# Optimization experiments

Hardware: AMD Instinct MI355X
Metric: run time of the kernel (lower is better)

Reference implementation:

```python
import jax, jax.numpy as jnp
import numpy as np

B, T, C = 4, 2048, 1024
N_HEAD = 16
HEAD = C // N_HEAD  # 64


def setup_inputs() -> dict:
    key = jax.random.key(0)
    k1, k2, k3 = jax.random.split(key, 3)
    x = jax.random.normal(k1, (B, T, C), dtype=jnp.float32)
    w_attn = jax.random.normal(k2, (C, 3 * C), dtype=jnp.float32) * (1.0 / np.sqrt(C))
    w_proj = jax.random.normal(k3, (C, C), dtype=jnp.float32) * (1.0 / np.sqrt(C))
    return {"x": x, "w_attn": w_attn, "w_proj": w_proj}


def reference(x, w_attn, w_proj):
    b, t, c = x.shape
    qkv = x @ w_attn  # [B,T,3C]
    q, k, v = jnp.split(qkv, 3, axis=-1)
    # [B,T,H,D] -> [B,H,T,D]
    q = q.reshape(b, t, N_HEAD, HEAD).transpose(0, 2, 1, 3)
    k = k.reshape(b, t, N_HEAD, HEAD).transpose(0, 2, 1, 3)
    v = v.reshape(b, t, N_HEAD, HEAD).transpose(0, 2, 1, 3)
    scale = 1.0 / np.sqrt(HEAD).astype(np.float32)
    attn = jnp.einsum('bhqd,bhkd->bhqk', q, k) * scale  # [B,H,T,T]
    causal = jnp.tril(jnp.ones((t, t), dtype=bool))
    attn = jnp.where(causal[None, None], attn, -jnp.inf)
    sm = jax.nn.softmax(attn, axis=-1)
    out = jnp.einsum('bhqk,bhkd->bhqd', sm, v)  # [B,H,T,D]
    out = out.transpose(0, 2, 1, 3).reshape(b, t, c)
    return out @ w_proj
```

## Files before the change

### kernel.cpp

```cpp
#include <hip/hip_runtime.h>
#include <stdint.h>

typedef unsigned short u16;
typedef __bf16 bf16x8 __attribute__((ext_vector_type(8)));
typedef float f32x4 __attribute__((ext_vector_type(4)));
typedef float f32x16 __attribute__((ext_vector_type(16)));

#define B_ 4
#define T_ 2048
#define C_ 1024
#define NH_ 16
#define HD_ 64
#define M_ (B_ * T_)
#define N1_ (3 * C_)
#define NQK_ 2048

__device__ inline u16 f2bf(float f) {
    uint32_t u = __float_as_uint(f);
    u += 0x7FFFu + ((u >> 16) & 1u);
    return (u16)(u >> 16);
}

__device__ inline bf16x8 ld_bf16x8(const u16* p) {
    return *(const bf16x8*)(const void*)p;
}

__device__ inline uint32_t cvtpk_bf16(float a, float b) {
    uint32_t r;
    asm("v_cvt_pk_bf16_f32 %0, %1, %2" : "=v"(r) : "v"(a), "v"(b));
    return r;
}

__device__ inline float exp2_fast(float x) {
    float r;
    asm("v_exp_f32 %0, %1" : "=v"(r) : "v"(x));
    return r;
}

__device__ inline void gload16(const u16* g, u16* l) {
    __builtin_amdgcn_global_load_lds(
        (const __attribute__((address_space(1))) uint32_t*)g,
        (__attribute__((address_space(3))) uint32_t*)l, 16, 0, 0);
}

__global__ void f32_to_bf16_k(const float* __restrict__ in, u16* __restrict__ out, int n) {
    int i = (blockIdx.x * blockDim.x + threadIdx.x) * 4;
    int stride = gridDim.x * blockDim.x * 4;
    for (; i < n; i += stride) {
        float4 v = *(const float4*)(in + i);
        uint2 o;
        o.x = (uint32_t)f2bf(v.x) | ((uint32_t)f2bf(v.y) << 16);
        o.y = (uint32_t)f2bf(v.z) | ((uint32_t)f2bf(v.w) << 16);
        *(uint2*)(out + i) = o;
    }
}

__global__ void transpose_f32_bf16_k(const float* __restrict__ in, u16* __restrict__ out,
                                     int R, int Cc, int scaleRows, float scale) {
    __shared__ float tile[32][33];
    int c0 = blockIdx.x * 32, r0 = blockIdx.y * 32;
    int tx = threadIdx.x, ty = threadIdx.y;
#pragma unroll
    for (int i = 0; i < 4; ++i)
        tile[ty + i * 8][tx] = in[(size_t)(r0 + ty + i * 8) * Cc + c0 + tx];
    __syncthreads();
#pragma unroll
    for (int i = 0; i < 4; ++i) {
        int orow = c0 + ty + i * 8;
        float v = tile[tx][ty + i * 8];
        if (orow < scaleRows) v *= scale;
        out[(size_t)orow * R + r0 + tx] = f2bf(v);
    }
}

template <int MODE>
__global__ __launch_bounds__(256) void gemm_bt_k(const u16* __restrict__ A,
                                                 const u16* __restrict__ Bt,
                                                 void* __restrict__ Cp,
                                                 u16* __restrict__ Vp,
                                                 int M, int N, int K) {
    __shared__ u16 As[3][128 * 32];
    __shared__ u16 Bs[3][128 * 32];
    const int t = threadIdx.x;
    const int w = t >> 6, l = t & 63;
    const int wr = w >> 1, wc = w & 1;
    const int lr = l & 15, lg = l >> 4;
    const int bid = blockIdx.x;
    const int xcd = bid & 7, j = bid >> 3;
    const int mt = xcd * 8 + (j & 7);
    const int nt = j >> 3;
    const int R0 = mt * 128, C0 = nt * 128;

    const int sr = t >> 2;
    const int sc = (((t & 3) ^ ((t >> 3) & 3)) * 8);
    const u16* Ag  = A  + (size_t)(R0 + sr) * K + sc;
    const u16* Ag2 = Ag + (size_t)64 * K;
    const u16* Bg  = Bt + (size_t)(C0 + sr) * K + sc;
    const u16* Bg2 = Bg + (size_t)64 * K;

    f32x4 acc[4][4] = {};
    const int nk = K / 32;

#define STAGE(KT, BI)                                               \
    do {                                                            \
        gload16(Ag  + (size_t)(KT) * 32, As[BI] + t * 8);           \
        gload16(Ag2 + (size_t)(KT) * 32, As[BI] + t * 8 + 2048);    \
        gload16(Bg  + (size_t)(KT) * 32, Bs[BI] + t * 8);           \
        gload16(Bg2 + (size_t)(KT) * 32, Bs[BI] + t * 8 + 2048);    \
    } while (0)

    STAGE(0, 0);
    if (nk > 1) STAGE(1, 1);

    const int lg8 = (lg * 8) ^ (((lr >> 1) & 3) * 8);

    int bi = 0;
    for (int kt = 0; kt < nk; ++kt) {
        if (kt + 1 < nk) asm volatile("s_waitcnt vmcnt(4)" ::: "memory");
        else             asm volatile("s_waitcnt vmcnt(0)" ::: "memory");
        __builtin_amdgcn_s_barrier();
        __builtin_amdgcn_sched_barrier(0);
        if (kt + 2 < nk) {
            int bn = bi + 2; if (bn >= 3) bn -= 3;
            STAGE(kt + 2, bn);
        }

        const u16* Ab = As[bi];
        const u16* Bb = Bs[bi];
        bf16x8 af[4], bfr[4];
#pragma unroll
        for (int mi = 0; mi < 4; ++mi)
            af[mi] = ld_bf16x8(Ab + (wr * 64 + mi * 16 + lr) * 32 + lg8);
#pragma unroll
        for (int nj = 0; nj < 4; ++nj)
            bfr[nj] = ld_bf16x8(Bb + (wc * 64 + nj * 16 + lr) * 32 + lg8);
        __builtin_amdgcn_s_setprio(1);
#pragma unroll
        for (int mi = 0; mi < 4; ++mi)
#pragma unroll
            for (int nj = 0; nj < 4; ++nj)
                acc[mi][nj] = __builtin_amdgcn_mfma_f32_16x16x32_bf16(af[mi], bfr[nj],
                                                                      acc[mi][nj], 0, 0, 0);
        __builtin_amdgcn_s_setprio(0);
        bi = (bi + 1 == 3) ? 0 : bi + 1;
    }
#undef STAGE

    if (MODE == 2 && C0 >= 2048) {
#pragma unroll
        for (int mi = 0; mi < 4; ++mi) {
            int row = R0 + wr * 64 + mi * 16 + lg * 4;
            int bb = row >> 11, tt = row & 2047;
#pragma unroll
            for (int nj = 0; nj < 4; ++nj) {
                int cv = C0 - 2048 + wc * 64 + nj * 16 + lr;
                int hh = cv >> 6, dd = cv & 63;
                ushort4 pk;
                pk.x = f2bf(acc[mi][nj][0]);
                pk.y = f2bf(acc[mi][nj][1]);
                pk.z = f2bf(acc[mi][nj][2]);
                pk.w = f2bf(acc[mi][nj][3]);
                *(ushort4*)(Vp + (((size_t)bb * NH_ + hh) * HD_ + dd) * (size_t)T_ + tt) = pk;
            }
        }
    } else {
#pragma unroll
        for (int mi = 0; mi < 4; ++mi) {
            int row = R0 + wr * 64 + mi * 16 + lg * 4;
#pragma unroll
            for (int nj = 0; nj < 4; ++nj) {
                int col = C0 + wc * 64 + nj * 16 + lr;
#pragma unroll
                for (int r = 0; r < 4; ++r) {
                    if (MODE == 0)
                        ((float*)Cp)[(size_t)(row + r) * N + col] = acc[mi][nj][r];
                    else
                        ((u16*)Cp)[(size_t)(row + r) * NQK_ + col] = f2bf(acc[mi][nj][r]);
                }
            }
        }
    }
}

__global__ __launch_bounds__(256, 3) void attn_fwd_k(const u16* __restrict__ qk,
                                                     const u16* __restrict__ vT,
                                                     u16* __restrict__ attO) {
    __shared__ u16 Ks[2][64 * 64];
    __shared__ u16 Vs[2][64 * 64];

    const int t = threadIdx.x;
    const int w = t >> 6, l = t & 63;
    const int r0 = l & 31, hi = l >> 5;
    const int lin = blockIdx.x;
    const int bh = (lin & 7) * 8 + ((lin >> 3) & 7);
    const int J = 15 - (lin >> 6);
    const int b = bh >> 4, h = bh & 15;
    const u16* qkB = qk + (size_t)b * T_ * NQK_;

    const int sr = t >> 3;
    const int sof = ((t & 7) * 8) ^ ((sr & 7) << 3);
    const u16* gK = qkB + (size_t)sr * NQK_ + C_ + h * HD_ + sof;
    const u16* gV = vT + ((size_t)bh * HD_ + sr) * (size_t)T_ + sof;

    const int qW = J * 128 + w * 32;
    const int nt = 2 * J + 2;

    bf16x8 qf[4];
    {
        const u16* qp = qkB + (size_t)(qW + r0) * NQK_ + h * HD_ + hi * 8;
#pragma unroll
        for (int dc = 0; dc < 4; ++dc) qf[dc] = ld_bf16x8(qp + dc * 16);
    }

    f32x16 acc0 = {}, acc1 = {};
    float m = -1e30f, lsum = 0.f;

    gload16(gK, Ks[0] + t * 8);
    gload16(gK + (size_t)32 * NQK_, Ks[0] + t * 8 + 2048);
    gload16(gV, Vs[0] + t * 8);
    gload16(gV + (size_t)32 * T_, Vs[0] + t * 8 + 2048);
    __syncthreads();

    for (int kt = 0; kt < nt; ++kt) {
        const int kv = kt * 64;
        if (kt + 1 < nt) {
            u16* dK = Ks[(kt + 1) & 1];
            u16* dV = Vs[(kt + 1) & 1];
            gload16(gK + (size_t)(kv + 64) * NQK_, dK + t * 8);
            gload16(gK + (size_t)(kv + 96) * NQK_, dK + t * 8 + 2048);
            gload16(gV + (kv + 64), dV + t * 8);
            gload16(gV + (size_t)32 * T_ + (kv + 64), dV + t * 8 + 2048);
        }
        const u16* Kb = Ks[kt & 1];
        const u16* Vb = Vs[kt & 1];

        if (kv <= qW) {
            const bool diag = (kv + 64 > qW);
            const bool up = (!diag) || (w & 1);

            f32x16 s0 = {}, s1 = {};
            __builtin_amdgcn_s_setprio(1);
#pragma unroll
            for (int dc = 0; dc < 4; ++dc) {
                int off = (dc * 32 + hi * 16) ^ ((r0 & 7) << 4);
                bf16x8 k0 = ld_bf16x8((const u16*)((const char*)Kb + r0 * 128 + off));
                s0 = __builtin_amdgcn_mfma_f32_32x32x16_bf16(k0, qf[dc], s0, 0, 0, 0);
                if (up) {
                    bf16x8 k1 = ld_bf16x8((const u16*)((const char*)Kb + r0 * 128 + 4096 + off));
                    s1 = __builtin_amdgcn_mfma_f32_32x32x16_bf16(k1, qf[dc], s1, 0, 0, 0);
                }
            }
            __builtin_amdgcn_s_setprio(0);

            if (diag) {
                int qrel = qW + r0 - kv;
#pragma unroll
                for (int rg = 0; rg < 16; ++rg) {
                    int kv0 = (rg & 3) + 8 * (rg >> 2) + hi * 4;
                    s0[rg] = (kv0 > qrel) ? -1e30f : s0[rg];
                    if (up) s1[rg] = (kv0 + 32 > qrel) ? -1e30f : s1[rg];
                }
            }

            float a4[8];
            if (up) {
#pragma unroll
                for (int i = 0; i < 8; ++i)
                    a4[i] = fmaxf(fmaxf(s0[i], s0[i + 8]), fmaxf(s1[i], s1[i + 8]));
            } else {
#pragma unroll
                for (int i = 0; i < 8; ++i) a4[i] = fmaxf(s0[i], s0[i + 8]);
            }
#pragma unroll
            for (int i = 0; i < 4; ++i) a4[i] = fmaxf(a4[i], a4[i + 4]);
            float mx = fmaxf(fmaxf(a4[0], a4[1]), fmaxf(a4[2], a4[3]));
            mx = fmaxf(mx, __shfl_xor(mx, 32));

            if (!__all(mx - m <= 8.f)) {
                float mn = fmaxf(m, mx);
                float corr = exp2_fast(m - mn);
                m = mn;
                lsum *= corr;
#pragma unroll
                for (int rg = 0; rg < 16; ++rg) { acc0[rg] *= corr; acc1[rg] *= corr; }
            }
#pragma unroll
            for (int rg = 0; rg < 16; ++rg) s0[rg] = exp2_fast(s0[rg] - m);
            if (up) {
#pragma unroll
                for (int rg = 0; rg < 16; ++rg) s1[rg] = exp2_fast(s1[rg] - m);
            }
            float sb[8];
            if (up) {
#pragma unroll
                for (int i = 0; i < 8; ++i) sb[i] = (s0[i] + s0[i + 8]) + (s1[i] + s1[i + 8]);
            } else {
#pragma unroll
                for (int i = 0; i < 8; ++i) sb[i] = s0[i] + s0[i + 8];
            }
#pragma unroll
            for (int i = 0; i < 4; ++i) sb[i] += sb[i + 4];
            float rs = (sb[0] + sb[1]) + (sb[2] + sb[3]);
            rs += __shfl_xor(rs, 32);
            lsum += rs;

            bf16x8 pb0, pb1, pb2, pb3;
            {
                uint32_t c0 = cvtpk_bf16(s0[0], s0[1]),   c1 = cvtpk_bf16(s0[2], s0[3]);
                uint32_t c2 = cvtpk_bf16(s0[4], s0[5]),   c3 = cvtpk_bf16(s0[6], s0[7]);
                uint32_t c4 = cvtpk_bf16(s0[8], s0[9]),   c5 = cvtpk_bf16(s0[10], s0[11]);
                uint32_t c6 = cvtpk_bf16(s0[12], s0[13]), c7 = cvtpk_bf16(s0[14], s0[15]);
                uint32_t x0 = (uint32_t)__shfl_xor((int)c0, 32), x1 = (uint32_t)__shfl_xor((int)c1, 32);
                uint32_t x2 = (uint32_t)__shfl_xor((int)c2, 32), x3 = (uint32_t)__shfl_xor((int)c3, 32);
                uint32_t x4 = (uint32_t)__shfl_xor((int)c4, 32), x5 = (uint32_t)__shfl_xor((int)c5, 32);
                uint32_t x6 = (uint32_t)__shfl_xor((int)c6, 32), x7 = (uint32_t)__shfl_xor((int)c7, 32);
                union { uint32_t u[4]; bf16x8 v; } f0, f1;
                f0.u[0] = hi ? x2 : c0;  f0.u[1] = hi ? x3 : c1;
                f0.u[2] = hi ? c2 : x0;  f0.u[3] = hi ? c3 : x1;
                f1.u[0] = hi ? x6 : c4;  f1.u[1] = hi ? x7 : c5;
                f1.u[2] = hi ? c6 : x4;  f1.u[3] = hi ? c7 : x5;
                pb0 = f0.v; pb1 = f1.v;
            }
            if (up) {
                uint32_t c0 = cvtpk_bf16(s1[0], s1[1]),   c1 = cvtpk_bf16(s1[2], s1[3]);
                uint32_t c2 = cvtpk_bf16(s1[4], s1[5]),   c3 = cvtpk_bf16(s1[6], s1[7]);
                uint32_t c4 = cvtpk_bf16(s1[8], s1[9]),   c5 = cvtpk_bf16(s1[10], s1[11]);
                uint32_t c6 = cvtpk_bf16(s1[12], s1[13]), c7 = cvtpk_bf16(s1[14], s1[15]);
                uint32_t x0 = (uint32_t)__shfl_xor((int)c0, 32), x1 = (uint32_t)__shfl_xor((int)c1, 32);
                uint32_t x2 = (uint32_t)__shfl_xor((int)c2, 32), x3 = (uint32_t)__shfl_xor((int)c3, 32);
                uint32_t x4 = (uint32_t)__shfl_xor((int)c4, 32), x5 = (uint32_t)__shfl_xor((int)c5, 32);
                uint32_t x6 = (uint32_t)__shfl_xor((int)c6, 32), x7 = (uint32_t)__shfl_xor((int)c7, 32);
                union { uint32_t u[4]; bf16x8 v; } f0, f1;
                f0.u[0] = hi ? x2 : c0;  f0.u[1] = hi ? x3 : c1;
                f0.u[2] = hi ? c2 : x0;  f0.u[3] = hi ? c3 : x1;
                f1.u[0] = hi ? x6 : c4;  f1.u[1] = hi ? x7 : c5;
                f1.u[2] = hi ? c6 : x4;  f1.u[3] = hi ? c7 : x5;
                pb2 = f0.v; pb3 = f1.v;
            }

            __builtin_amdgcn_s_setprio(1);
            {
                int off0 = (hi * 16) ^ ((r0 & 7) << 4);
                int off1 = (32 + hi * 16) ^ ((r0 & 7) << 4);
                bf16x8 va0 = ld_bf16x8((const u16*)((const char*)Vb + r0 * 128 + off0));
                bf16x8 va1 = ld_bf16x8((const u16*)((const char*)Vb + r0 * 128 + off1));
                bf16x8 vb0 = ld_bf16x8((const u16*)((const char*)Vb + r0 * 128 + 4096 + off0));
                bf16x8 vb1 = ld_bf16x8((const u16*)((const char*)Vb + r0 * 128 + 4096 + off1));
                acc0 = __builtin_amdgcn_mfma_f32_32x32x16_bf16(va0, pb0, acc0, 0, 0, 0);
                acc0 = __builtin_amdgcn_mfma_f32_32x32x16_bf16(va1, pb1, acc0, 0, 0, 0);
                acc1 = __builtin_amdgcn_mfma_f32_32x32x16_bf16(vb0, pb0, acc1, 0, 0, 0);
                acc1 = __builtin_amdgcn_mfma_f32_32x32x16_bf16(vb1, pb1, acc1, 0, 0, 0);
                if (up) {
                    int off2 = (64 + hi * 16) ^ ((r0 & 7) << 4);
                    int off3 = (96 + hi * 16) ^ ((r0 & 7) << 4);
                    bf16x8 va2 = ld_bf16x8((const u16*)((const char*)Vb + r0 * 128 + off2));
                    bf16x8 va3 = ld_bf16x8((const u16*)((const char*)Vb + r0 * 128 + off3));
                    bf16x8 vb2 = ld_bf16x8((const u16*)((const char*)Vb + r0 * 128 + 4096 + off2));
                    bf16x8 vb3 = ld_bf16x8((const u16*)((const char*)Vb + r0 * 128 + 4096 + off3));
                    acc0 = __builtin_amdgcn_mfma_f32_32x32x16_bf16(va2, pb2, acc0, 0, 0, 0);
                    acc0 = __builtin_amdgcn_mfma_f32_32x32x16_bf16(va3, pb3, acc0, 0, 0, 0);
                    acc1 = __builtin_amdgcn_mfma_f32_32x32x16_bf16(vb2, pb2, acc1, 0, 0, 0);
                    acc1 = __builtin_amdgcn_mfma_f32_32x32x16_bf16(vb3, pb3, acc1, 0, 0, 0);
                }
            }
            __builtin_amdgcn_s_setprio(0);
        }

        __syncthreads();
    }

    float inv = 1.0f / lsum;
    u16* op = attO + ((size_t)b * T_ + qW + r0) * C_ + h * HD_;
#pragma unroll
    for (int g = 0; g < 4; ++g) {
        int d0 = g * 8 + hi * 4;
        ushort4 p0, p1;
        p0.x = f2bf(acc0[4 * g + 0] * inv);
        p0.y = f2bf(acc0[4 * g + 1] * inv);
        p0.z = f2bf(acc0[4 * g + 2] * inv);
        p0.w = f2bf(acc0[4 * g + 3] * inv);
        *(ushort4*)(op + d0) = p0;
        p1.x = f2bf(acc1[4 * g + 0] * inv);
        p1.y = f2bf(acc1[4 * g + 1] * inv);
        p1.z = f2bf(acc1[4 * g + 2] * inv);
        p1.w = f2bf(acc1[4 * g + 3] * inv);
        *(ushort4*)(op + 32 + d0) = p1;
    }
}

extern "C" void kernel_launch(void* const* d_in, const int* in_sizes, int n_in,
                              void* d_out, int out_size, void* d_ws, size_t ws_size,
                              hipStream_t stream) {
    const float* x      = (const float*)d_in[0];
    const float* w_attn = (const float*)d_in[1];
    const float* w_proj = (const float*)d_in[2];
    float* out = (float*)d_out;

    char* ws = (char*)d_ws;
    const size_t SZ_XB = (size_t)M_ * C_ * 2;
    const size_t SZ_WA = (size_t)C_ * N1_ * 2;
    const size_t SZ_WP = (size_t)C_ * C_ * 2;
    const size_t SZ_QK = (size_t)M_ * NQK_ * 2;
    const size_t SZ_VT = (size_t)M_ * C_ * 2;
    u16* xb   = (u16*)ws;
    u16* waT  = (u16*)(ws + SZ_XB);
    u16* wpT  = (u16*)(ws + SZ_XB + SZ_WA);
    u16* qkb  = (u16*)(ws + SZ_XB + SZ_WA + SZ_WP);
    u16* vtb  = (u16*)(ws + SZ_XB + SZ_WA + SZ_WP + SZ_QK);
    u16* attO = (u16*)(ws + SZ_XB + SZ_WA + SZ_WP + SZ_QK + SZ_VT);

    f32_to_bf16_k<<<2048, 256, 0, stream>>>(x, xb, M_ * C_);
    dim3 tb(32, 8);
    transpose_f32_bf16_k<<<dim3(N1_ / 32, C_ / 32), tb, 0, stream>>>(w_attn, waT, C_, N1_, C_,
                                                                     0.125f * 1.44269504088896f);
    transpose_f32_bf16_k<<<dim3(C_ / 32, C_ / 32), tb, 0, stream>>>(w_proj, wpT, C_, C_, 0, 1.0f);

    gemm_bt_k<2><<<dim3((M_ / 128) * (N1_ / 128)), 256, 0, stream>>>(xb, waT, qkb, vtb, M_, N1_, C_);
    attn_fwd_k<<<dim3(1024), 256, 0, stream>>>(qkb, vtb, attO);
    gemm_bt_k<0><<<dim3((M_ / 128) * (C_ / 128)), 256, 0, stream>>>(attO, wpT, out, nullptr, M_, C_, C_);
}
```

Before: 184.3 us.

## Split GEMM A/B staging with shallower B prefetch and nontemporal epilogue stores

The GEMM now triple-buffers the A tile two iterations ahead but double-buffers the B tile only one iteration ahead, which shrinks LDS use and loosens the vmcnt wait to two outstanding loads. Epilogue stores (fp32 output, bf16 qk, transposed V) become nontemporal, and the V store packs its values into two 32-bit words. The aim is lower LDS pressure for better occupancy and less cache pollution from streaming outputs. The risk is that B loads have less time to land before use, which can expose memory latency, and that nontemporal stores may hurt when the attention kernel rereads qk and V soon after.

```diff
diff --git a/kernel.cpp b/kernel.cpp
--- a/kernel.cpp
+++ b/kernel.cpp
@@ -5,6 +5,7 @@
 typedef __bf16 bf16x8 __attribute__((ext_vector_type(8)));
 typedef float f32x4 __attribute__((ext_vector_type(4)));
 typedef float f32x16 __attribute__((ext_vector_type(16)));
+typedef unsigned int u32x2 __attribute__((ext_vector_type(2)));
 
 #define B_ 4
 #define T_ 2048
@@ -80,7 +81,7 @@
                                                  u16* __restrict__ Vp,
                                                  int M, int N, int K) {
     __shared__ u16 As[3][128 * 32];
-    __shared__ u16 Bs[3][128 * 32];
+    __shared__ u16 Bs[2][128 * 32];
     const int t = threadIdx.x;
     const int w = t >> 6, l = t & 63;
     const int wr = w >> 1, wc = w & 1;
@@ -101,32 +102,36 @@
     f32x4 acc[4][4] = {};
     const int nk = K / 32;
 
-#define STAGE(KT, BI)                                               \
+#define STAGE_A(KT, BI)                                             \
     do {                                                            \
         gload16(Ag  + (size_t)(KT) * 32, As[BI] + t * 8);           \
         gload16(Ag2 + (size_t)(KT) * 32, As[BI] + t * 8 + 2048);    \
+    } while (0)
+#define STAGE_B(KT, BI)                                             \
+    do {                                                            \
         gload16(Bg  + (size_t)(KT) * 32, Bs[BI] + t * 8);           \
         gload16(Bg2 + (size_t)(KT) * 32, Bs[BI] + t * 8 + 2048);    \
     } while (0)
 
-    STAGE(0, 0);
-    if (nk > 1) STAGE(1, 1);
+    STAGE_A(0, 0);
+    STAGE_B(0, 0);
+    if (nk > 1) STAGE_A(1, 1);
 
     const int lg8 = (lg * 8) ^ (((lr >> 1) & 3) * 8);
 
-    int bi = 0;
     for (int kt = 0; kt < nk; ++kt) {
-        if (kt + 1 < nk) asm volatile("s_waitcnt vmcnt(4)" ::: "memory");
+        if (kt + 1 < nk) asm volatile("s_waitcnt vmcnt(2)" ::: "memory");
         else             asm volatile("s_waitcnt vmcnt(0)" ::: "memory");
         __builtin_amdgcn_s_barrier();
         __builtin_amdgcn_sched_barrier(0);
+        if (kt + 1 < nk) STAGE_B(kt + 1, (kt + 1) & 1);
         if (kt + 2 < nk) {
-            int bn = bi + 2; if (bn >= 3) bn -= 3;
-            STAGE(kt + 2, bn);
+            int an = kt + 2; an -= (an / 3) * 3;
+            STAGE_A(kt + 2, an);
         }
 
-        const u16* Ab = As[bi];
-        const u16* Bb = Bs[bi];
+        const u16* Ab = As[kt % 3];
+        const u16* Bb = Bs[kt & 1];
         bf16x8 af[4], bfr[4];
 #pragma unroll
         for (int mi = 0; mi < 4; ++mi)
@@ -142,9 +147,9 @@
                 acc[mi][nj] = __builtin_amdgcn_mfma_f32_16x16x32_bf16(af[mi], bfr[nj],
                                                                       acc[mi][nj], 0, 0, 0);
         __builtin_amdgcn_s_setprio(0);
-        bi = (bi + 1 == 3) ? 0 : bi + 1;
-    }
-#undef STAGE
+    }
+#undef STAGE_A
+#undef STAGE_B
 
     if (MODE == 2 && C0 >= 2048) {
 #pragma unroll
@@ -155,12 +160,11 @@
             for (int nj = 0; nj < 4; ++nj) {
                 int cv = C0 - 2048 + wc * 64 + nj * 16 + lr;
                 int hh = cv >> 6, dd = cv & 63;
-                ushort4 pk;
-                pk.x = f2bf(acc[mi][nj][0]);
-                pk.y = f2bf(acc[mi][nj][1]);
-                pk.z = f2bf(acc[mi][nj][2]);
-                pk.w = f2bf(acc[mi][nj][3]);
-                *(ushort4*)(Vp + (((size_t)bb * NH_ + hh) * HD_ + dd) * (size_t)T_ + tt) = pk;
+                u32x2 pk;
+                pk.x = (uint32_t)f2bf(acc[mi][nj][0]) | ((uint32_t)f2bf(acc[mi][nj][1]) << 16);
+                pk.y = (uint32_t)f2bf(acc[mi][nj][2]) | ((uint32_t)f2bf(acc[mi][nj][3]) << 16);
+                __builtin_nontemporal_store(
+                    pk, (u32x2*)(Vp + (((size_t)bb * NH_ + hh) * HD_ + dd) * (size_t)T_ + tt));
             }
         }
     } else {
@@ -173,9 +177,11 @@
 #pragma unroll
                 for (int r = 0; r < 4; ++r) {
                     if (MODE == 0)
-                        ((float*)Cp)[(size_t)(row + r) * N + col] = acc[mi][nj][r];
+                        __builtin_nontemporal_store(acc[mi][nj][r],
+                                                    &((float*)Cp)[(size_t)(row + r) * N + col]);
                     else
-                        ((u16*)Cp)[(size_t)(row + r) * NQK_ + col] = f2bf(acc[mi][nj][r]);
+                        __builtin_nontemporal_store(f2bf(acc[mi][nj][r]),
+                                                    &((u16*)Cp)[(size_t)(row + r) * NQK_ + col]);
                 }
             }
         }
```

Measured after the change: 208.7 us. 13.3% more time.
